# Kernel optimization log

Measured on AMD Instinct MI355X. Metric: run time of the kernel, lower is better.

## Reference

```python
import jax, jax.numpy as jnp
import numpy as np

N = 100000   # nodes
E = 1600000  # edges
DIN = 100    # input feature dim
D = 64       # hidden dim per GCN layer
G = 512      # graphs in batch
EPS = 1e-5


def setup_inputs() -> dict:
    key = jax.random.key(0)
    ks = jax.random.split(key, 16)
    inp = {}
    inp["x"] = jax.random.normal(ks[0], (N, DIN), dtype=jnp.float32)
    inp["edge_index"] = jax.random.randint(ks[1], (2, E), 0, N)
    inp["edge_weight"] = jax.random.uniform(ks[2], (E,), dtype=jnp.float32)
    inp["batch"] = jnp.sort(jax.random.randint(ks[3], (N,), 0, G))
    dims = [DIN, D, D, D]
    for i in range(3):
        fan_in = dims[i]
        inp[f"w{i}"] = jax.random.normal(ks[4 + i], (dims[i], dims[i + 1]), dtype=jnp.float32) / np.sqrt(fan_in)
        inp[f"b{i}"] = jnp.zeros((dims[i + 1],), dtype=jnp.float32)
        inp[f"g{i}"] = jnp.ones((dims[i + 1],), dtype=jnp.float32)   # BN scale
        inp[f"be{i}"] = jnp.zeros((dims[i + 1],), dtype=jnp.float32)  # BN shift
    inp["out_w"] = jax.random.normal(ks[7], (D, 1), dtype=jnp.float32) / np.sqrt(D)
    inp["out_b"] = jnp.zeros((1,), dtype=jnp.float32)
    return inp


def reference(x, edge_index, edge_weight, batch,
              w0, b0, g0, be0, w1, b1, g1, be1, w2, b2, g2, be2,
              out_w, out_b):
    src, dst = edge_index[0], edge_index[1]
    n = x.shape[0]
    # GCN symmetric normalization with self-loops (PyG gcn_norm, fill_value=1)
    deg = jnp.zeros((n,), dtype=x.dtype).at[dst].add(edge_weight) + 1.0
    dinv = jax.lax.rsqrt(deg)
    norm = edge_weight * dinv[src] * dinv[dst]   # [E]
    self_coeff = dinv * dinv                      # 1/deg, self-loop norm  [N]

    def gcn_bn_relu(h, w, b, g, be):
        h = h @ w + b                                             # linear transform [N,D]
        msg = norm[:, None] * h[src]                              # gather + weight [E,D]
        agg = jnp.zeros_like(h).at[dst].add(msg) + h * self_coeff[:, None]
        mean = agg.mean(axis=0)
        var = agg.var(axis=0)                                     # biased var (torch BN)
        hn = (agg - mean) * jax.lax.rsqrt(var + EPS) * g + be
        return jax.nn.relu(hn)                                    # dropout p=0 -> identity

    h = gcn_bn_relu(x, w0, b0, g0, be0)
    h = gcn_bn_relu(h, w1, b1, g1, be1)
    h = gcn_bn_relu(h, w2, b2, g2, be2)

    # global mean pool per graph
    sums = jax.ops.segment_sum(h, batch, num_segments=G)
    counts = jax.ops.segment_sum(jnp.ones((n, 1), dtype=h.dtype), batch, num_segments=G)
    pooled = sums / jnp.maximum(counts, 1.0)
    return pooled @ out_w + out_b
```

## Files before the change

kernel.cpp:

```cpp
#include <hip/hip_runtime.h>
#include <hip/hip_fp16.h>
#include <cstdint>

#define DH 64
#define EPSV 1e-5f
#define GBLK 2048
#define NBUK 256
#define BROWS 512
#define BINJ 8
#define CAP 12288

typedef _Float16 half8 __attribute__((ext_vector_type(8)));
typedef float f32x4 __attribute__((ext_vector_type(4)));

__global__ void k_fill(float* __restrict__ p, float v, size_t n) {
  size_t i = blockIdx.x * (size_t)blockDim.x + threadIdx.x;
  if (i < n) p[i] = v;
}

__global__ void k_gcur0(unsigned* __restrict__ gcur0) {
  gcur0[threadIdx.x] = (unsigned)(threadIdx.x * CAP);
}

__global__ __launch_bounds__(256) void k_xhalf(const float* __restrict__ x,
                                               unsigned short* __restrict__ xh,
                                               int N_, int K) {
  const int cpr = K / 4;
  size_t i = blockIdx.x * 256ull + threadIdx.x;
  if (i >= (size_t)N_ * cpr) return;
  int row = (int)(i / cpr), c0 = (int)(i % cpr) * 4;
  float4 v = *(const float4*)&x[(size_t)row * K + c0];
  ushort4 h;
  h.x = __half_as_ushort(__float2half(v.x));
  h.y = __half_as_ushort(__float2half(v.y));
  h.z = __half_as_ushort(__float2half(v.z));
  h.w = __half_as_ushort(__float2half(v.w));
  *(ushort4*)&xh[(size_t)row * 128 + c0] = h;
  if (c0 == K - 4) {
    ushort4 z4 = {0, 0, 0, 0};
    uint4 z16 = {0, 0, 0, 0};
    *(ushort4*)&xh[(size_t)row * 128 + K] = z4;
    *(uint4*)&xh[(size_t)row * 128 + K + 4] = z16;
    *(uint4*)&xh[(size_t)row * 128 + K + 12] = z16;
    *(uint4*)&xh[(size_t)row * 128 + K + 20] = z16;
  }
}

__global__ void k_wt(const float* __restrict__ W, unsigned short* __restrict__ wt,
                     int Kreal, int KP) {
  int idx = blockIdx.x * 256 + threadIdx.x;
  if (idx >= 64 * KP) return;
  int c = idx / KP, k = idx % KP;
  float v = (k < Kreal) ? W[k * DH + c] : 0.f;
  wt[idx] = __half_as_ushort(__float2half(v));
}

__global__ __launch_bounds__(256) void k_bin0(
    const int* __restrict__ src, const int* __restrict__ dst,
    const float* __restrict__ ew, unsigned* __restrict__ gcur0,
    unsigned long long* __restrict__ bstage, int E_) {
  __shared__ unsigned cntL[NBUK], offL[NBUK], runL[NBUK];
  const int t = threadIdx.x;
  const int base = blockIdx.x * (256 * BINJ);
  cntL[t] = 0;
  runL[t] = 0;
  __syncthreads();
  unsigned hi[BINJ], lo[BINJ];
  int bb[BINJ];
#pragma unroll
  for (int j = 0; j < BINJ; ++j) {
    int e = base + j * 256 + t;
    bb[j] = -1;
    if (e < E_) {
      int q = dst[e];
      hi[j] = ((unsigned)(q & (BROWS - 1)) << 17) | (unsigned)src[e];
      lo[j] = __float_as_uint(ew[e]);
      bb[j] = q >> 9;
      atomicAdd(&cntL[bb[j]], 1u);
    }
  }
  __syncthreads();
  offL[t] = cntL[t] ? atomicAdd(&gcur0[t], cntL[t]) : 0u;
  __syncthreads();
#pragma unroll
  for (int j = 0; j < BINJ; ++j) {
    if (bb[j] >= 0) {
      unsigned p = offL[bb[j]] + atomicAdd(&runL[bb[j]], 1u);
      bstage[p] = ((unsigned long long)hi[j] << 32) | lo[j];
    }
  }
}

__global__ __launch_bounds__(256) void k_bcnt(
    const unsigned long long* __restrict__ bstage, const unsigned* __restrict__ gcur0,
    int* __restrict__ cnt, float* __restrict__ dinv, float* __restrict__ sc, int N_) {
  __shared__ unsigned cntL[BROWS], degL[BROWS];
  const int b = blockIdx.x, t = threadIdx.x;
  for (int i = t; i < BROWS; i += 256) {
    cntL[i] = 0;
    degL[i] = 0;
  }
  __syncthreads();
  const unsigned beg = (unsigned)(b * CAP), end = gcur0[b];
  for (unsigned p = beg + t; p < end; p += 256) {
    unsigned long long v = bstage[p];
    unsigned r = (unsigned)(v >> 49);
    float w = __uint_as_float((unsigned)v);
    atomicAdd(&cntL[r], 1u);
    atomicAdd(&degL[r], (unsigned)(w * 16777216.0f));
  }
  __syncthreads();
  for (int i = t; i < BROWS; i += 256) {
    int r = b * BROWS + i;
    if (r < N_) {
      float deg = 1.0f + (float)degL[i] * (1.0f / 16777216.0f);
      cnt[r] = (int)cntL[i];
      dinv[r] = rsqrtf(deg);
      sc[r] = 1.0f / deg;
    }
  }
}

__global__ __launch_bounds__(256) void k_scan1(const int* __restrict__ cnt,
                                               int* __restrict__ out,
                                               int* __restrict__ bsums,
                                               int N_, int n1) {
  __shared__ int sm[256];
  const int t = threadIdx.x;
  const int base = blockIdx.x * 1024 + t * 4;
  int v[4], lsum = 0;
#pragma unroll
  for (int j = 0; j < 4; ++j) {
    int i = base + j;
    v[j] = (i < N_) ? ((cnt[i] + 7) & ~7) : 0;
    lsum += v[j];
  }
  sm[t] = lsum;
  __syncthreads();
  for (int o = 1; o < 256; o <<= 1) {
    int x = (t >= o) ? sm[t - o] : 0;
    __syncthreads();
    if (t >= o) sm[t] += x;
    __syncthreads();
  }
  int run = sm[t] - lsum;
#pragma unroll
  for (int j = 0; j < 4; ++j) {
    int i = base + j;
    if (i < n1) out[i] = run;
    run += v[j];
  }
  if (t == 255) bsums[blockIdx.x] = sm[255];
}

__global__ __launch_bounds__(256) void k_scan2(int* __restrict__ bsums, int nb) {
  __shared__ int sm[256];
  int t = threadIdx.x;
  int v = (t < nb) ? bsums[t] : 0;
  sm[t] = v;
  __syncthreads();
  for (int o = 1; o < 256; o <<= 1) {
    int x = (t >= o) ? sm[t - o] : 0;
    __syncthreads();
    if (t >= o) sm[t] += x;
    __syncthreads();
  }
  if (t < nb) bsums[t] = sm[t] - v;
}

__global__ void k_scan3(int* __restrict__ out, const int* __restrict__ bsums, int n1) {
  int i = blockIdx.x * blockDim.x + threadIdx.x;
  if (i < n1) out[i] += bsums[i >> 10];
}

__global__ __launch_bounds__(256) void k_fin(
    const unsigned long long* __restrict__ bstage, const int* __restrict__ rowstart,
    const unsigned* __restrict__ gcur0, const float* __restrict__ dinv,
    unsigned* __restrict__ elist, int N_) {
  __shared__ unsigned lcur[BROWS];
  __shared__ int rsL[BROWS + 1];
  __shared__ float dvL[BROWS];
  const int b = blockIdx.x, t = threadIdx.x;
  const int r0 = b * BROWS;
  for (int i = t; i < BROWS; i += 256) {
    lcur[i] = 0;
    int r = r0 + i;
    dvL[i] = (r < N_) ? dinv[r] : 0.f;
  }
  for (int i = t; i <= BROWS; i += 256) {
    int r = r0 + i;
    if (r > N_) r = N_;
    rsL[i] = rowstart[r];
  }
  __syncthreads();
  const unsigned beg = (unsigned)(b * CAP), end = gcur0[b];
  for (unsigned p = beg + t; p < end; p += 256) {
    unsigned long long v = bstage[p];
    unsigned hi = (unsigned)(v >> 32);
    unsigned r = hi >> 17;
    unsigned s = hi & 0x1FFFFu;
    float w = __uint_as_float((unsigned)v);
    float nm = w * dinv[s] * dvL[r];
    unsigned h15 = (unsigned)__half_as_ushort(__float2half(nm));
    unsigned slot = (unsigned)rsL[r] + atomicAdd(&lcur[r], 1u);
    elist[slot] = (h15 << 17) | s;
  }
  __syncthreads();
  for (int i = t; i < BROWS; i += 256) {
    unsigned p = (unsigned)rsL[i] + lcur[i];
    const unsigned pe = (unsigned)rsL[i + 1];
    for (; p < pe; ++p) elist[p] = 0u;
  }
}

__global__ void k_gbound(const int* __restrict__ batch, int* __restrict__ gstart,
                         int N_, int G_) {
  int i = blockIdx.x * blockDim.x + threadIdx.x;
  if (i >= N_) return;
  int b = batch[i];
  if (i == 0) {
    for (int g = 0; g <= b; ++g) gstart[g] = 0;
  }
  int nb = (i + 1 < N_) ? batch[i + 1] : G_;
  for (int g = b + 1; g <= nb; ++g) gstart[g] = i + 1;
}

template <int KP, int FUSE>
__global__ __launch_bounds__(256) void k_gemm_mfma(
    const unsigned short* __restrict__ Aa, const unsigned short* __restrict__ wt,
    const float* __restrict__ bias, const float* __restrict__ stats,
    const float* __restrict__ gam, const float* __restrict__ bet,
    __half* __restrict__ Hh, int n, float invN) {
  __shared__ unsigned short Ah[128 * KP];
  __shared__ unsigned short Bt[64 * KP];
  __shared__ float saL[DH], sbL[DH];
  const int tid = threadIdx.x;
  const int r0 = blockIdx.x * 128;
  if (FUSE) {
    if (tid < DH) {
      float mean = stats[tid] * invN;
      float var = stats[DH + tid] * invN - mean * mean;
      float a = rsqrtf(var + EPSV) * gam[tid];
      saL[tid] = a;
      sbL[tid] = bet[tid] - mean * a;
    }
    __syncthreads();
  }
  constexpr int KC = KP / 8;
  for (int ci = tid; ci < 128 * KC; ci += 256) {
    int row = ci / KC, kc = ci % KC, k0 = kc * 8;
    int gr = r0 + row;
    uint4 av = {0, 0, 0, 0};
    if (gr < n) av = *(const uint4*)&Aa[(size_t)gr * KP + k0];
    if (FUSE) {
      const unsigned short* ap = (const unsigned short*)&av;
      unsigned short ov[8];
#pragma unroll
      for (int j = 0; j < 8; ++j) {
        int k = k0 + j;
        float a = __half2float(__ushort_as_half(ap[j]));
        ov[j] = __half_as_ushort(__float2half(fmaxf(a * saL[k] + sbL[k], 0.f)));
      }
      av = *(uint4*)ov;
    }
    *(uint4*)&Ah[row * KP + (k0 ^ ((row & 7) * 8))] = av;
  }
  for (int ci = tid; ci < 64 * KC; ci += 256) {
    int c = ci / KC, kc = ci % KC, k0 = kc * 8;
    uint4 wv = *(const uint4*)&wt[c * KP + k0];
    *(uint4*)&Bt[c * KP + (k0 ^ ((c & 7) * 8))] = wv;
  }
  __syncthreads();
  const int w = tid >> 6, l = tid & 63;
  const int lr = l & 15, lg = l >> 4;
  f32x4 acc[2][4];
#pragma unroll
  for (int a1 = 0; a1 < 2; ++a1)
#pragma unroll
    for (int a2 = 0; a2 < 4; ++a2) acc[a1][a2] = (f32x4){0.f, 0.f, 0.f, 0.f};
#pragma unroll
  for (int ks = 0; ks < KP / 32; ++ks) {
    const int k0 = ks * 32 + lg * 8;
    half8 av[2], bv[4];
#pragma unroll
    for (int rf = 0; rf < 2; ++rf) {
      int row = w * 32 + rf * 16 + lr;
      av[rf] = *(const half8*)&Ah[row * KP + (k0 ^ ((row & 7) * 8))];
    }
#pragma unroll
    for (int cf = 0; cf < 4; ++cf) {
      int col = cf * 16 + lr;
      bv[cf] = *(const half8*)&Bt[col * KP + (k0 ^ ((col & 7) * 8))];
    }
#pragma unroll
    for (int rf = 0; rf < 2; ++rf)
#pragma unroll
      for (int cf = 0; cf < 4; ++cf)
        acc[rf][cf] =
            __builtin_amdgcn_mfma_f32_16x16x32_f16(av[rf], bv[cf], acc[rf][cf], 0, 0, 0);
  }
  unsigned short* Hu = (unsigned short*)Hh;
#pragma unroll
  for (int rf = 0; rf < 2; ++rf) {
#pragma unroll
    for (int cf = 0; cf < 4; ++cf) {
      int col = cf * 16 + lr;
      float bcol = bias[col];
#pragma unroll
      for (int i = 0; i < 4; ++i) {
        int row = r0 + w * 32 + rf * 16 + lg * 4 + i;
        if (row < n)
          Hu[(size_t)row * DH + col] = __half_as_ushort(__float2half(acc[rf][cf][i] + bcol));
      }
    }
  }
}

__global__ __launch_bounds__(256) void k_gather(
    const unsigned* __restrict__ elist, const int* __restrict__ rowstart,
    const __half* __restrict__ Hh, const float* __restrict__ sc,
    __half* __restrict__ AGGh, float* __restrict__ statp, int n) {
  const int wid = threadIdx.x >> 6;
  const int d = threadIdx.x & 63;
  const int gw = blockIdx.x * 4 + wid;
  const int nw = gridDim.x * 4;
  unsigned short* AGGu = (unsigned short*)AGGh;
  float s = 0.f, ss = 0.f;
  for (int row = gw; row < n; row += nw) {
    const int rs = rowstart[row], re = rowstart[row + 1];
    float acc = __half2float(Hh[(size_t)row * DH + d]) * sc[row];
    for (int base = rs; base < re; base += 64) {
      const int rem = re - base;
      unsigned eL = 0u;
      if (d < rem) eL = __builtin_nontemporal_load(&elist[base + d]);
      const int m = rem < 64 ? rem : 64;
      for (int j = 0; j < m; j += 8) {
#pragma unroll
        for (int jj = 0; jj < 8; ++jj) {
          const unsigned e = __shfl(eL, j + jj, 64);
          const float v = __half2float(Hh[(size_t)(e & 0x1FFFFu) * DH + d]);
          const float nm =
              __half2float(__ushort_as_half((unsigned short)(e >> 17)));
          acc = fmaf(nm, v, acc);
        }
      }
    }
    __builtin_nontemporal_store(__half_as_ushort(__float2half(acc)),
                                &AGGu[(size_t)row * DH + d]);
    s += acc;
    ss += acc * acc;
  }
  __shared__ float sm[4][DH], sm2[4][DH];
  sm[wid][d] = s;
  sm2[wid][d] = ss;
  __syncthreads();
  if (threadIdx.x < DH) {
    float a = sm[0][d] + sm[1][d] + sm[2][d] + sm[3][d];
    float b = sm2[0][d] + sm2[1][d] + sm2[2][d] + sm2[3][d];
    __builtin_nontemporal_store(a, &statp[(size_t)blockIdx.x * 128 + d]);
    __builtin_nontemporal_store(b, &statp[(size_t)blockIdx.x * 128 + DH + d]);
  }
}

__global__ __launch_bounds__(256) void k_redstats(const float* __restrict__ statp,
                                                  float* __restrict__ stats, int nblk) {
  const int t = blockIdx.x;
  float s = 0.f;
  for (int b = threadIdx.x; b < nblk; b += 256) s += statp[(size_t)b * 128 + t];
#pragma unroll
  for (int o = 32; o > 0; o >>= 1) s += __shfl_down(s, o, 64);
  __shared__ float sm[4];
  if ((threadIdx.x & 63) == 0) sm[threadIdx.x >> 6] = s;
  __syncthreads();
  if (threadIdx.x == 0) stats[t] = sm[0] + sm[1] + sm[2] + sm[3];
}

__global__ __launch_bounds__(256) void k_poolhead(
    const __half* __restrict__ AGGh, const float* __restrict__ stats,
    const float* __restrict__ gam, const float* __restrict__ bet,
    const float* __restrict__ ow, const int* __restrict__ gstart,
    const float* __restrict__ ob, float* __restrict__ out, float invN) {
  const int g = blockIdx.x;
  const int gs = gstart[g], ge = gstart[g + 1];
  const int wid = threadIdx.x >> 6;
  const int d = threadIdx.x & 63;
  float mean = stats[d] * invN;
  float var = stats[DH + d] * invN - mean * mean;
  float sa = rsqrtf(var + EPSV) * gam[d];
  float sb = bet[d] - mean * sa;
  const float w = ow[d];
  float acc = 0.f;
  for (int row = gs + wid; row < ge; row += 4)
    acc += fmaxf(__half2float(AGGh[(size_t)row * DH + d]) * sa + sb, 0.f) * w;
#pragma unroll
  for (int off = 32; off > 0; off >>= 1) acc += __shfl_down(acc, off, 64);
  __shared__ float sm[4];
  if (d == 0) sm[wid] = acc;
  __syncthreads();
  if (threadIdx.x == 0) {
    float s = sm[0] + sm[1] + sm[2] + sm[3];
    float cnt = (float)(ge - gs);
    out[g] = s / fmaxf(cnt, 1.0f) + ob[0];
  }
}

extern "C" void kernel_launch(void* const* d_in, const int* in_sizes, int n_in,
                              void* d_out, int out_size, void* d_ws, size_t ws_size,
                              hipStream_t stream) {
  const float* x    = (const float*)d_in[0];
  const int*   ei   = (const int*)d_in[1];
  const float* ew   = (const float*)d_in[2];
  const int*   batch= (const int*)d_in[3];
  const float* w0   = (const float*)d_in[4];
  const float* b0   = (const float*)d_in[5];
  const float* g0   = (const float*)d_in[6];
  const float* be0  = (const float*)d_in[7];
  const float* w1   = (const float*)d_in[8];
  const float* b1   = (const float*)d_in[9];
  const float* g1   = (const float*)d_in[10];
  const float* be1  = (const float*)d_in[11];
  const float* w2   = (const float*)d_in[12];
  const float* b2   = (const float*)d_in[13];
  const float* g2   = (const float*)d_in[14];
  const float* be2  = (const float*)d_in[15];
  const float* ow   = (const float*)d_in[16];
  const float* ob   = (const float*)d_in[17];

  const int N_  = in_sizes[3];
  const int E_  = in_sizes[2];
  const int DIN_= in_sizes[0] / N_;
  const int G_  = out_size;
  const int* srcIdx = ei;
  const int* dstIdx = ei + E_;
  const int n1 = N_ + 1;
  const size_t epad = (size_t)E_ + 7ull * N_;

  float* ws = (float*)d_ws;
  size_t off = 0;
  unsigned long long* bstage = (unsigned long long*)(ws + off);
  off += (size_t)2 * NBUK * CAP;
  unsigned* elist = (unsigned*)(ws + off); off += epad;
  float* dinv     = ws + off; off += N_;
  float* sc       = ws + off; off += N_;
  int*   cnt      = (int*)(ws + off); off += N_;
  int*   rowstart = (int*)(ws + off); off += n1 + 1;
  int*   bsums    = (int*)(ws + off); off += 256;
  unsigned* gcur0 = (unsigned*)(ws + off); off += NBUK;
  int*   gstart   = (int*)(ws + off); off += G_ + 1;
  __half* hhalf   = (__half*)(ws + off); off += (size_t)N_ * DH / 2;
  __half* aggh    = (__half*)(ws + off); off += (size_t)N_ * DH / 2;
  unsigned short* xh = (unsigned short*)(ws + off); off += (size_t)N_ * 64;
  unsigned short* wt0 = (unsigned short*)(ws + off); off += 64 * 128 / 2;
  unsigned short* wt1 = (unsigned short*)(ws + off); off += 64 * 64 / 2;
  unsigned short* wt2 = (unsigned short*)(ws + off); off += 64 * 64 / 2;
  float* stats    = ws + off; off += 2 * DH;
  float* statp    = ws + off; off += (size_t)GBLK * 128;
  (void)ws_size; (void)n_in;

  k_xhalf<<<(int)(((size_t)N_ * (DIN_ / 4) + 255) / 256), 256, 0, stream>>>(x, xh, N_, DIN_);
  k_wt<<<(64 * 128 + 255) / 256, 256, 0, stream>>>(w0, wt0, DIN_, 128);
  k_wt<<<(64 * 64 + 255) / 256, 256, 0, stream>>>(w1, wt1, DH, 64);
  k_wt<<<(64 * 64 + 255) / 256, 256, 0, stream>>>(w2, wt2, DH, 64);

  k_gcur0<<<1, NBUK, 0, stream>>>(gcur0);
  k_bin0<<<(E_ + 256 * BINJ - 1) / (256 * BINJ), 256, 0, stream>>>(
      srcIdx, dstIdx, ew, gcur0, bstage, E_);
  k_bcnt<<<NBUK, 256, 0, stream>>>(bstage, gcur0, cnt, dinv, sc, N_);

  const int nb = (n1 + 1023) / 1024;
  k_scan1<<<nb, 256, 0, stream>>>(cnt, rowstart, bsums, N_, n1);
  k_scan2<<<1, 256, 0, stream>>>(bsums, nb);
  k_scan3<<<(n1 + 255) / 256, 256, 0, stream>>>(rowstart, bsums, n1);

  k_fin<<<NBUK, 256, 0, stream>>>(bstage, rowstart, gcur0, dinv, elist, N_);

  k_gbound<<<(N_ + 255) / 256, 256, 0, stream>>>(batch, gstart, N_, G_);

  const float* Bl[3]  = {b0, b1, b2};
  const float* Gl[3]  = {g0, g1, g2};
  const float* BeL[3] = {be0, be1, be2};
  const unsigned short* Wt[3] = {wt0, wt1, wt2};

  const float invN = 1.0f / (float)N_;
  const int gblk = (N_ + 127) / 128;

  for (int l = 0; l < 3; ++l) {
    if (l == 0) {
      k_gemm_mfma<128, 0><<<gblk, 256, 0, stream>>>(
          xh, Wt[0], Bl[0], stats, nullptr, nullptr, hhalf, N_, invN);
    } else {
      k_gemm_mfma<64, 1><<<gblk, 256, 0, stream>>>(
          (const unsigned short*)aggh, Wt[l], Bl[l], stats, Gl[l - 1], BeL[l - 1],
          hhalf, N_, invN);
    }
    k_gather<<<GBLK, 256, 0, stream>>>(elist, rowstart, hhalf, sc, aggh, statp, N_);
    k_redstats<<<128, 256, 0, stream>>>(statp, stats, GBLK);
  }

  k_poolhead<<<G_, 256, 0, stream>>>(aggh, stats, g2, be2, ow, gstart, ob,
                                     (float*)d_out, invN);
}
```

Baseline: 338.2 us.

## Split hidden features into two 32-column halves and gather each half separately

```diff
diff --git a/kernel.cpp b/kernel.cpp
--- a/kernel.cpp
+++ b/kernel.cpp
@@ -12,11 +12,6 @@
 
 typedef _Float16 half8 __attribute__((ext_vector_type(8)));
 typedef float f32x4 __attribute__((ext_vector_type(4)));
-
-__global__ void k_fill(float* __restrict__ p, float v, size_t n) {
-  size_t i = blockIdx.x * (size_t)blockDim.x + threadIdx.x;
-  if (i < n) p[i] = v;
-}
 
 __global__ void k_gcur0(unsigned* __restrict__ gcur0) {
   gcur0[threadIdx.x] = (unsigned)(threadIdx.x * CAP);
@@ -132,7 +127,7 @@
 #pragma unroll
   for (int j = 0; j < 4; ++j) {
     int i = base + j;
-    v[j] = (i < N_) ? ((cnt[i] + 7) & ~7) : 0;
+    v[j] = (i < N_) ? cnt[i] : 0;
     lsum += v[j];
   }
   sm[t] = lsum;
@@ -178,7 +173,7 @@
     const unsigned* __restrict__ gcur0, const float* __restrict__ dinv,
     unsigned* __restrict__ elist, int N_) {
   __shared__ unsigned lcur[BROWS];
-  __shared__ int rsL[BROWS + 1];
+  __shared__ int rsL[BROWS];
   __shared__ float dvL[BROWS];
   const int b = blockIdx.x, t = threadIdx.x;
   const int r0 = b * BROWS;
@@ -186,11 +181,7 @@
     lcur[i] = 0;
     int r = r0 + i;
     dvL[i] = (r < N_) ? dinv[r] : 0.f;
-  }
-  for (int i = t; i <= BROWS; i += 256) {
-    int r = r0 + i;
-    if (r > N_) r = N_;
-    rsL[i] = rowstart[r];
+    rsL[i] = (r < N_) ? rowstart[r] : 0;
   }
   __syncthreads();
   const unsigned beg = (unsigned)(b * CAP), end = gcur0[b];
@@ -205,12 +196,6 @@
     unsigned slot = (unsigned)rsL[r] + atomicAdd(&lcur[r], 1u);
     elist[slot] = (h15 << 17) | s;
   }
-  __syncthreads();
-  for (int i = t; i < BROWS; i += 256) {
-    unsigned p = (unsigned)rsL[i] + lcur[i];
-    const unsigned pe = (unsigned)rsL[i + 1];
-    for (; p < pe; ++p) elist[p] = 0u;
-  }
 }
 
 __global__ void k_gbound(const int* __restrict__ batch, int* __restrict__ gstart,
@@ -227,10 +212,11 @@
 
 template <int KP, int FUSE>
 __global__ __launch_bounds__(256) void k_gemm_mfma(
-    const unsigned short* __restrict__ Aa, const unsigned short* __restrict__ wt,
-    const float* __restrict__ bias, const float* __restrict__ stats,
-    const float* __restrict__ gam, const float* __restrict__ bet,
-    __half* __restrict__ Hh, int n, float invN) {
+    const unsigned short* __restrict__ A0, const unsigned short* __restrict__ A1,
+    const unsigned short* __restrict__ wt, const float* __restrict__ bias,
+    const float* __restrict__ stats, const float* __restrict__ gam,
+    const float* __restrict__ bet, unsigned short* __restrict__ Hu0,
+    unsigned short* __restrict__ Hu1, int n, float invN) {
   __shared__ unsigned short Ah[128 * KP];
   __shared__ unsigned short Bt[64 * KP];
   __shared__ float saL[DH], sbL[DH];
@@ -251,7 +237,14 @@
     int row = ci / KC, kc = ci % KC, k0 = kc * 8;
     int gr = r0 + row;
     uint4 av = {0, 0, 0, 0};
-    if (gr < n) av = *(const uint4*)&Aa[(size_t)gr * KP + k0];
+    if (gr < n) {
+      if (FUSE) {
+        const unsigned short* P = (kc < KC / 2) ? A0 : A1;
+        av = *(const uint4*)&P[(size_t)gr * 32 + (k0 & 31)];
+      } else {
+        av = *(const uint4*)&A0[(size_t)gr * KP + k0];
+      }
+    }
     if (FUSE) {
       const unsigned short* ap = (const unsigned short*)&av;
       unsigned short ov[8];
@@ -299,66 +292,80 @@
         acc[rf][cf] =
             __builtin_amdgcn_mfma_f32_16x16x32_f16(av[rf], bv[cf], acc[rf][cf], 0, 0, 0);
   }
-  unsigned short* Hu = (unsigned short*)Hh;
 #pragma unroll
   for (int rf = 0; rf < 2; ++rf) {
 #pragma unroll
     for (int cf = 0; cf < 4; ++cf) {
       int col = cf * 16 + lr;
       float bcol = bias[col];
+      unsigned short* Hp = (col < 32) ? Hu0 : Hu1;
 #pragma unroll
       for (int i = 0; i < 4; ++i) {
         int row = r0 + w * 32 + rf * 16 + lg * 4 + i;
         if (row < n)
-          Hu[(size_t)row * DH + col] = __half_as_ushort(__float2half(acc[rf][cf][i] + bcol));
+          Hp[(size_t)row * 32 + (col & 31)] =
+              __half_as_ushort(__float2half(acc[rf][cf][i] + bcol));
       }
     }
   }
 }
 
-__global__ __launch_bounds__(256) void k_gather(
+__global__ __launch_bounds__(256) void k_gather2(
     const unsigned* __restrict__ elist, const int* __restrict__ rowstart,
-    const __half* __restrict__ Hh, const float* __restrict__ sc,
-    __half* __restrict__ AGGh, float* __restrict__ statp, int n) {
+    const unsigned short* __restrict__ Hp, const float* __restrict__ sc,
+    unsigned short* __restrict__ AGGp, float* __restrict__ statp, int n, int pofs) {
   const int wid = threadIdx.x >> 6;
-  const int d = threadIdx.x & 63;
+  const int lane = threadIdx.x & 63;
+  const int d = lane & 31;
+  const int h = lane >> 5;
   const int gw = blockIdx.x * 4 + wid;
   const int nw = gridDim.x * 4;
-  unsigned short* AGGu = (unsigned short*)AGGh;
   float s = 0.f, ss = 0.f;
   for (int row = gw; row < n; row += nw) {
     const int rs = rowstart[row], re = rowstart[row + 1];
-    float acc = __half2float(Hh[(size_t)row * DH + d]) * sc[row];
+    float acc = (h == 0)
+        ? __half2float(__ushort_as_half(Hp[(size_t)row * 32 + d])) * sc[row]
+        : 0.f;
     for (int base = rs; base < re; base += 64) {
       const int rem = re - base;
       unsigned eL = 0u;
-      if (d < rem) eL = __builtin_nontemporal_load(&elist[base + d]);
-      const int m = rem < 64 ? rem : 64;
+      if (lane < rem) eL = __builtin_nontemporal_load(&elist[base + lane]);
+      const int m = rem < 64 ? ((rem + 7) & ~7) : 64;
       for (int j = 0; j < m; j += 8) {
-#pragma unroll
-        for (int jj = 0; jj < 8; ++jj) {
-          const unsigned e = __shfl(eL, j + jj, 64);
-          const float v = __half2float(Hh[(size_t)(e & 0x1FFFFu) * DH + d]);
-          const float nm =
-              __half2float(__ushort_as_half((unsigned short)(e >> 17)));
-          acc = fmaf(nm, v, acc);
+        unsigned e[4];
+        float v[4];
+#pragma unroll
+        for (int jj = 0; jj < 4; ++jj) e[jj] = __shfl(eL, j + jj * 2 + h, 64);
+#pragma unroll
+        for (int jj = 0; jj < 4; ++jj)
+          v[jj] = __half2float(__ushort_as_half(Hp[(size_t)(e[jj] & 0x1FFFFu) * 32 + d]));
+#pragma unroll
+        for (int jj = 0; jj < 4; ++jj) {
+          float nm = __half2float(__ushort_as_half((unsigned short)(e[jj] >> 17)));
+          acc = fmaf(nm, v[jj], acc);
         }
       }
     }
-    __builtin_nontemporal_store(__half_as_ushort(__float2half(acc)),
-                                &AGGu[(size_t)row * DH + d]);
-    s += acc;
-    ss += acc * acc;
-  }
-  __shared__ float sm[4][DH], sm2[4][DH];
-  sm[wid][d] = s;
-  sm2[wid][d] = ss;
-  __syncthreads();
-  if (threadIdx.x < DH) {
+    float other = __shfl_down(acc, 32, 64);
+    if (h == 0) {
+      float full = acc + other;
+      __builtin_nontemporal_store(__half_as_ushort(__float2half(full)),
+                                  &AGGp[(size_t)row * 32 + d]);
+      s += full;
+      ss += full * full;
+    }
+  }
+  __shared__ float sm[4][32], sm2[4][32];
+  if (h == 0) {
+    sm[wid][d] = s;
+    sm2[wid][d] = ss;
+  }
+  __syncthreads();
+  if (threadIdx.x < 32) {
     float a = sm[0][d] + sm[1][d] + sm[2][d] + sm[3][d];
     float b = sm2[0][d] + sm2[1][d] + sm2[2][d] + sm2[3][d];
-    __builtin_nontemporal_store(a, &statp[(size_t)blockIdx.x * 128 + d]);
-    __builtin_nontemporal_store(b, &statp[(size_t)blockIdx.x * 128 + DH + d]);
+    __builtin_nontemporal_store(a, &statp[(size_t)blockIdx.x * 128 + pofs + d]);
+    __builtin_nontemporal_store(b, &statp[(size_t)blockIdx.x * 128 + 64 + pofs + d]);
   }
 }
 
@@ -376,10 +383,11 @@
 }
 
 __global__ __launch_bounds__(256) void k_poolhead(
-    const __half* __restrict__ AGGh, const float* __restrict__ stats,
-    const float* __restrict__ gam, const float* __restrict__ bet,
-    const float* __restrict__ ow, const int* __restrict__ gstart,
-    const float* __restrict__ ob, float* __restrict__ out, float invN) {
+    const unsigned short* __restrict__ A0, const unsigned short* __restrict__ A1,
+    const float* __restrict__ stats, const float* __restrict__ gam,
+    const float* __restrict__ bet, const float* __restrict__ ow,
+    const int* __restrict__ gstart, const float* __restrict__ ob,
+    float* __restrict__ out, float invN) {
   const int g = blockIdx.x;
   const int gs = gstart[g], ge = gstart[g + 1];
   const int wid = threadIdx.x >> 6;
@@ -389,9 +397,13 @@
   float sa = rsqrtf(var + EPSV) * gam[d];
   float sb = bet[d] - mean * sa;
   const float w = ow[d];
+  const unsigned short* P = (d < 32) ? A0 : A1;
+  const int dl = d & 31;
   float acc = 0.f;
-  for (int row = gs + wid; row < ge; row += 4)
-    acc += fmaxf(__half2float(AGGh[(size_t)row * DH + d]) * sa + sb, 0.f) * w;
+  for (int row = gs + wid; row < ge; row += 4) {
+    float v = __half2float(__ushort_as_half(P[(size_t)row * 32 + dl]));
+    acc += fmaxf(v * sa + sb, 0.f) * w;
+  }
 #pragma unroll
   for (int off = 32; off > 0; off >>= 1) acc += __shfl_down(acc, off, 64);
   __shared__ float sm[4];
@@ -433,13 +445,12 @@
   const int* srcIdx = ei;
   const int* dstIdx = ei + E_;
   const int n1 = N_ + 1;
-  const size_t epad = (size_t)E_ + 7ull * N_;
 
   float* ws = (float*)d_ws;
   size_t off = 0;
   unsigned long long* bstage = (unsigned long long*)(ws + off);
   off += (size_t)2 * NBUK * CAP;
-  unsigned* elist = (unsigned*)(ws + off); off += epad;
+  unsigned* elist = (unsigned*)(ws + off); off += E_;
   float* dinv     = ws + off; off += N_;
   float* sc       = ws + off; off += N_;
   int*   cnt      = (int*)(ws + off); off += N_;
@@ -447,8 +458,10 @@
   int*   bsums    = (int*)(ws + off); off += 256;
   unsigned* gcur0 = (unsigned*)(ws + off); off += NBUK;
   int*   gstart   = (int*)(ws + off); off += G_ + 1;
-  __half* hhalf   = (__half*)(ws + off); off += (size_t)N_ * DH / 2;
-  __half* aggh    = (__half*)(ws + off); off += (size_t)N_ * DH / 2;
+  unsigned short* h0   = (unsigned short*)(ws + off); off += (size_t)N_ * 16;
+  unsigned short* h1   = (unsigned short*)(ws + off); off += (size_t)N_ * 16;
+  unsigned short* agg0 = (unsigned short*)(ws + off); off += (size_t)N_ * 16;
+  unsigned short* agg1 = (unsigned short*)(ws + off); off += (size_t)N_ * 16;
   unsigned short* xh = (unsigned short*)(ws + off); off += (size_t)N_ * 64;
   unsigned short* wt0 = (unsigned short*)(ws + off); off += 64 * 128 / 2;
   unsigned short* wt1 = (unsigned short*)(ws + off); off += 64 * 64 / 2;
@@ -487,16 +500,16 @@
   for (int l = 0; l < 3; ++l) {
     if (l == 0) {
       k_gemm_mfma<128, 0><<<gblk, 256, 0, stream>>>(
-          xh, Wt[0], Bl[0], stats, nullptr, nullptr, hhalf, N_, invN);
+          xh, nullptr, Wt[0], Bl[0], stats, nullptr, nullptr, h0, h1, N_, invN);
     } else {
       k_gemm_mfma<64, 1><<<gblk, 256, 0, stream>>>(
-          (const unsigned short*)aggh, Wt[l], Bl[l], stats, Gl[l - 1], BeL[l - 1],
-          hhalf, N_, invN);
-    }
-    k_gather<<<GBLK, 256, 0, stream>>>(elist, rowstart, hhalf, sc, aggh, statp, N_);
+          agg0, agg1, Wt[l], Bl[l], stats, Gl[l - 1], BeL[l - 1], h0, h1, N_, invN);
+    }
+    k_gather2<<<GBLK, 256, 0, stream>>>(elist, rowstart, h0, sc, agg0, statp, N_, 0);
+    k_gather2<<<GBLK, 256, 0, stream>>>(elist, rowstart, h1, sc, agg1, statp, N_, 32);
     k_redstats<<<128, 256, 0, stream>>>(statp, stats, GBLK);
   }
 
-  k_poolhead<<<G_, 256, 0, stream>>>(aggh, stats, g2, be2, ow, gstart, ob,
+  k_poolhead<<<G_, 256, 0, stream>>>(agg0, agg1, stats, g2, be2, ow, gstart, ob,
                                      (float*)d_out, invN);
 }
```

After: 393.9 us. +16.5%, slower.
